# Optimization experiments

Measured on AMD Instinct MI355X. Metric: run time of the kernel, lower is better.

The kernel has to match this reference:

```python
import jax, jax.numpy as jnp
import numpy as np

MAXDISP = 48  # init kwarg
KS = list(range(3, 12))  # window sizes 3..11 -> channel prefixes k*k (9..121)


def setup_inputs() -> dict:
    key = jax.random.key(0)
    k1, k2 = jax.random.split(key)
    B, C, H, W = 2, 121, 128, 256
    x = jax.random.normal(k1, (B, C, H, W), dtype=jnp.float32)
    y = jax.random.normal(k2, (B, C, H, W), dtype=jnp.float32)
    return {"x": x, "y": y}


def reference(x, y):
    # GetCostVolume forward (attack=True branch: mean |x - shifted y| over
    # nested channel prefixes idx=k*k, k=3..11, for each disparity shift).
    # Note: the attack=False branch replaces |x-y| with (x!=y).float(); for
    # continuous random inputs that is identically 1, so we implement the
    # differentiable abs-diff branch, which has identical loop/memory structure.
    B, C, H, W = x.shape
    ksq = jnp.array([k * k for k in KS], dtype=x.dtype)          # (9,) divisors
    prefix_idx = jnp.array([k * k - 1 for k in KS])              # cumsum gather idx
    wpos = jnp.arange(W)

    def body(carry, d):
        # shift y right by d along width; region w<d is masked to zero below,
        # matching cost[..., :d] = 0 from the torch zeros-init.
        y_sh = jnp.roll(y, d, axis=-1)                           # (B,C,H,W)
        diff = jnp.abs(x - y_sh)                                 # (B,C,H,W)
        csum = jnp.cumsum(diff, axis=1)                          # prefix sums over channels
        means = csum[:, prefix_idx] / ksq[:, None, None]         # (B,9,H,W)
        means = jnp.where(wpos >= d, means, jnp.zeros((), x.dtype))
        return carry, means

    _, cost = jax.lax.scan(body, None, jnp.arange(MAXDISP))      # (D,B,9,H,W)
    return jnp.transpose(cost, (1, 2, 0, 3, 4))                  # (B,9,D,H,W)
```

## Files before the change

kernel.cpp:

```cpp
#include <hip/hip_runtime.h>

#define B_ 2
#define C_ 121
#define H_ 128
#define W_ 256
#define D_ 48
#define CT 11
#define NCHUNK 11
#define NT 256
#define NDY 4
#define ZS 3
#define XROW 264
#define YROW 312

constexpr int HW = H_ * W_;

typedef float f32x4 __attribute__((ext_vector_type(4)));
typedef const void __attribute__((address_space(1)))* gas1_t;
typedef void __attribute__((address_space(3)))* las3_t;

#define VMWAIT(NSTR) asm volatile("s_waitcnt vmcnt(" NSTR ")" ::: "memory")
#define CFENCE()     asm volatile("" ::: "memory")

__launch_bounds__(NT, 3)
__global__ void cost_volume_kernel(const float* __restrict__ xg,
                                   const float* __restrict__ yg,
                                   float* __restrict__ out)
{
    __shared__ __align__(16) float XLS[2][CT][XROW];
    __shared__ __align__(16) float YLS[2][CT][YROW];

    const int t  = threadIdx.x;
    const int h  = blockIdx.x;
    const int b  = blockIdx.y;
    const int z  = blockIdx.z;
    const int wq = t & 63;
    const int wv = t >> 6;
    const int d0 = z * 16 + wv * NDY;
    const int w0 = wq * 4;
    const int bp = w0 - d0 + 44;

    for (int i = t; i < 2 * CT * 48; i += NT) {
        int nb = i / (CT * 48);
        int r  = i % (CT * 48);
        YLS[nb][r / 48][r % 48] = 0.0f;
    }

    const size_t row0 = (((size_t)b * C_) * H_ + h) * (size_t)W_;
    const float* xrow = xg + row0 + (size_t)wq * 4;
    const float* yrow = yg + row0 + (size_t)wq * 4;

    auto stage = [&](int chunk, int nb) {
        for (int i = wv; i < 2 * CT; i += 4) {
            const int cc = i >> 1;
            const size_t off = (size_t)(chunk * CT + cc) * HW;
            if (i & 1)
                __builtin_amdgcn_global_load_lds((gas1_t)(yrow + off),
                                                 (las3_t)&YLS[nb][cc][48], 16, 0, 0);
            else
                __builtin_amdgcn_global_load_lds((gas1_t)(xrow + off),
                                                 (las3_t)&XLS[nb][cc][0], 16, 0, 0);
        }
    };

    stage(0, 0);
    stage(1, 1);

    float acc[NDY][4] = {};

    for (int k = 0; k < NCHUNK; ++k) {
        const int cur = k & 1;

        if (k < NCHUNK - 1) {
            if (wv < 2) VMWAIT("6"); else VMWAIT("5");
        } else {
            VMWAIT("0");
        }
        __builtin_amdgcn_s_barrier();
        CFENCE();

        #pragma unroll
        for (int cc = 0; cc < CT; ++cc) {
            const f32x4 xv = *(const f32x4*)&XLS[cur][cc][w0];
            float yw[8];
            *(f32x4*)&yw[0] = *(const f32x4*)&YLS[cur][cc][bp];
            *(f32x4*)&yw[4] = *(const f32x4*)&YLS[cur][cc][bp + 4];

            const float xvv[4] = {xv.x, xv.y, xv.z, xv.w};
            #pragma unroll
            for (int jd = 0; jd < NDY; ++jd)
                #pragma unroll
                for (int jw = 0; jw < 4; ++jw)
                    acc[jd][jw] += __builtin_fabsf(xvv[jw] - yw[4 + jw - jd]);

            #pragma unroll
            for (int bi = 0; bi < 9; ++bi) {
                constexpr int KB[9] = {8, 15, 24, 35, 48, 63, 80, 99, 120};
                if (k * CT + cc == KB[bi]) {
                    const float inv = 1.0f / (float)(KB[bi] + 1);
                    const size_t obase = (((size_t)b * 9 + bi) * D_) * (size_t)HW
                                       + (size_t)h * W_ + (size_t)w0;
                    #pragma unroll
                    for (int jd = 0; jd < NDY; ++jd) {
                        const int d = d0 + jd;
                        f32x4 v;
                        v.x = (w0 + 0 >= d) ? acc[jd][0] * inv : 0.0f;
                        v.y = (w0 + 1 >= d) ? acc[jd][1] * inv : 0.0f;
                        v.z = (w0 + 2 >= d) ? acc[jd][2] * inv : 0.0f;
                        v.w = (w0 + 3 >= d) ? acc[jd][3] * inv : 0.0f;
                        *(f32x4*)&out[obase + (size_t)d * HW] = v;
                    }
                }
            }
        }

        if (k + 2 < NCHUNK) {
            CFENCE();
            __builtin_amdgcn_s_barrier();
            stage(k + 2, cur);
        }
    }
}

extern "C" void kernel_launch(void* const* d_in, const int* in_sizes, int n_in,
                              void* d_out, int out_size, void* d_ws, size_t ws_size,
                              hipStream_t stream)
{
    const float* x = (const float*)d_in[0];
    const float* y = (const float*)d_in[1];
    float* o = (float*)d_out;
    dim3 grid(H_, B_, ZS);
    dim3 block(NT, 1, 1);
    hipLaunchKernelGGL(cost_volume_kernel, grid, block, 0, stream, x, y, o);
}
```

Baseline: 52.80 us.

## Switch to triple-buffered 7-channel chunks with single barrier per iteration

Shrinks the channel chunk from 11 to 7 and moves from double to triple LDS buffering. The next-but-one chunk is issued right after the barrier, so there is only one barrier per iteration instead of two, and loads overlap with compute. Per-iteration vmcnt waits are computed from a bitmask of which chunks issued output stores. The last two channels are handled by a special tail load. This adds more iterations, a fragile wait-count scheme and more LDS per block, which may hurt occupancy.

```diff
diff --git a/kernel.cpp b/kernel.cpp
--- a/kernel.cpp
+++ b/kernel.cpp
@@ -5,13 +5,14 @@
 #define H_ 128
 #define W_ 256
 #define D_ 48
-#define CT 11
-#define NCHUNK 11
+#define CT 7
+#define NFULL 17
 #define NT 256
 #define NDY 4
 #define ZS 3
 #define XROW 264
 #define YROW 312
+#define NBUF 3
 
 constexpr int HW = H_ * W_;
 
@@ -22,13 +23,26 @@
 #define VMWAIT(NSTR) asm volatile("s_waitcnt vmcnt(" NSTR ")" ::: "memory")
 #define CFENCE()     asm volatile("" ::: "memory")
 
+constexpr unsigned SBm = (1u<<1)|(1u<<2)|(1u<<3)|(1u<<5)|(1u<<6)|(1u<<9)|(1u<<11)|(1u<<14);
+
+__device__ __forceinline__ void vmwait_n(int n) {
+    switch (n) {
+        case 3:  VMWAIT("3");  break;
+        case 4:  VMWAIT("4");  break;
+        case 7:  VMWAIT("7");  break;
+        case 8:  VMWAIT("8");  break;
+        case 11: VMWAIT("11"); break;
+        default: VMWAIT("12"); break;
+    }
+}
+
 __launch_bounds__(NT, 3)
 __global__ void cost_volume_kernel(const float* __restrict__ xg,
                                    const float* __restrict__ yg,
                                    float* __restrict__ out)
 {
-    __shared__ __align__(16) float XLS[2][CT][XROW];
-    __shared__ __align__(16) float YLS[2][CT][YROW];
+    __shared__ __align__(16) float XLS[NBUF][CT][XROW];
+    __shared__ __align__(16) float YLS[NBUF][CT][YROW];
 
     const int t  = threadIdx.x;
     const int h  = blockIdx.x;
@@ -40,7 +54,7 @@
     const int w0 = wq * 4;
     const int bp = w0 - d0 + 44;
 
-    for (int i = t; i < 2 * CT * 48; i += NT) {
+    for (int i = t; i < NBUF * CT * 48; i += NT) {
         int nb = i / (CT * 48);
         int r  = i % (CT * 48);
         YLS[nb][r / 48][r % 48] = 0.0f;
@@ -62,64 +76,76 @@
                                                  (las3_t)&XLS[nb][cc][0], 16, 0, 0);
         }
     };
+    auto stage_tail = [&]() {
+        const int cc = wv >> 1;
+        const size_t off = (size_t)(119 + cc) * HW;
+        if (wv & 1)
+            __builtin_amdgcn_global_load_lds((gas1_t)(yrow + off),
+                                             (las3_t)&YLS[2][cc][48], 16, 0, 0);
+        else
+            __builtin_amdgcn_global_load_lds((gas1_t)(xrow + off),
+                                             (las3_t)&XLS[2][cc][0], 16, 0, 0);
+    };
+
+    float acc[NDY][4] = {};
+
+    auto chan = [&](int nb, int cc, int ch) {
+        const f32x4 xv = *(const f32x4*)&XLS[nb][cc][w0];
+        float yw[8];
+        *(f32x4*)&yw[0] = *(const f32x4*)&YLS[nb][cc][bp];
+        *(f32x4*)&yw[4] = *(const f32x4*)&YLS[nb][cc][bp + 4];
+        const float xvv[4] = {xv.x, xv.y, xv.z, xv.w};
+        #pragma unroll
+        for (int jd = 0; jd < NDY; ++jd)
+            #pragma unroll
+            for (int jw = 0; jw < 4; ++jw)
+                acc[jd][jw] += __builtin_fabsf(xvv[jw] - yw[4 + jw - jd]);
+
+        constexpr int KB[9] = {8, 15, 24, 35, 48, 63, 80, 99, 120};
+        #pragma unroll
+        for (int bi = 0; bi < 9; ++bi) {
+            if (ch == KB[bi]) {
+                const float inv = 1.0f / (float)(KB[bi] + 1);
+                const size_t obase = (((size_t)b * 9 + bi) * D_) * (size_t)HW
+                                   + (size_t)h * W_ + (size_t)w0;
+                #pragma unroll
+                for (int jd = 0; jd < NDY; ++jd) {
+                    const int d = d0 + jd;
+                    f32x4 v;
+                    v.x = (w0 + 0 >= d) ? acc[jd][0] * inv : 0.0f;
+                    v.y = (w0 + 1 >= d) ? acc[jd][1] * inv : 0.0f;
+                    v.z = (w0 + 2 >= d) ? acc[jd][2] * inv : 0.0f;
+                    v.w = (w0 + 3 >= d) ? acc[jd][3] * inv : 0.0f;
+                    *(f32x4*)&out[obase + (size_t)d * HW] = v;
+                }
+            }
+        }
+    };
 
     stage(0, 0);
     stage(1, 1);
 
-    float acc[NDY][4] = {};
-
-    for (int k = 0; k < NCHUNK; ++k) {
-        const int cur = k & 1;
-
-        if (k < NCHUNK - 1) {
-            if (wv < 2) VMWAIT("6"); else VMWAIT("5");
-        } else {
-            VMWAIT("0");
-        }
+    for (int k = 0; k < NFULL; ++k) {
+        const int nb = k % 3;
+        const int nw = (wv < 2 ? 4 : 3)
+                     + ((k >= 1 && ((SBm >> (k - 1)) & 1)) ? 4 : 0)
+                     + ((k >= 2 && ((SBm >> (k - 2)) & 1)) ? 4 : 0);
+        vmwait_n(nw);
         __builtin_amdgcn_s_barrier();
         CFENCE();
+        if (k + 2 < NFULL)       stage(k + 2, (k + 2) % 3);
+        else if (k + 2 == NFULL) stage_tail();
+        CFENCE();
+        #pragma unroll
+        for (int cc = 0; cc < CT; ++cc)
+            chan(nb, cc, k * CT + cc);
+    }
 
-        #pragma unroll
-        for (int cc = 0; cc < CT; ++cc) {
-            const f32x4 xv = *(const f32x4*)&XLS[cur][cc][w0];
-            float yw[8];
-            *(f32x4*)&yw[0] = *(const f32x4*)&YLS[cur][cc][bp];
-            *(f32x4*)&yw[4] = *(const f32x4*)&YLS[cur][cc][bp + 4];
-
-            const float xvv[4] = {xv.x, xv.y, xv.z, xv.w};
-            #pragma unroll
-            for (int jd = 0; jd < NDY; ++jd)
-                #pragma unroll
-                for (int jw = 0; jw < 4; ++jw)
-                    acc[jd][jw] += __builtin_fabsf(xvv[jw] - yw[4 + jw - jd]);
-
-            #pragma unroll
-            for (int bi = 0; bi < 9; ++bi) {
-                constexpr int KB[9] = {8, 15, 24, 35, 48, 63, 80, 99, 120};
-                if (k * CT + cc == KB[bi]) {
-                    const float inv = 1.0f / (float)(KB[bi] + 1);
-                    const size_t obase = (((size_t)b * 9 + bi) * D_) * (size_t)HW
-                                       + (size_t)h * W_ + (size_t)w0;
-                    #pragma unroll
-                    for (int jd = 0; jd < NDY; ++jd) {
-                        const int d = d0 + jd;
-                        f32x4 v;
-                        v.x = (w0 + 0 >= d) ? acc[jd][0] * inv : 0.0f;
-                        v.y = (w0 + 1 >= d) ? acc[jd][1] * inv : 0.0f;
-                        v.z = (w0 + 2 >= d) ? acc[jd][2] * inv : 0.0f;
-                        v.w = (w0 + 3 >= d) ? acc[jd][3] * inv : 0.0f;
-                        *(f32x4*)&out[obase + (size_t)d * HW] = v;
-                    }
-                }
-            }
-        }
-
-        if (k + 2 < NCHUNK) {
-            CFENCE();
-            __builtin_amdgcn_s_barrier();
-            stage(k + 2, cur);
-        }
-    }
+    VMWAIT("0");
+    __builtin_amdgcn_s_barrier();
+    CFENCE();
+    chan(2, 0, 119);
+    chan(2, 1, 120);
 }
 
 extern "C" void kernel_launch(void* const* d_in, const int* in_sizes, int n_in,
```

New measurement: 59.24 us. 12.2% more time.
